# Kernel optimization log

Hardware: AMD Instinct MI355X
Metric: run time of the kernel (lower is better)

Reference implementation:

```python
import jax, jax.numpy as jnp
import numpy as np

B, T, N, E, H, MAXD = 32, 128, 42, 256, 8, 7
DH = E // H


def _hand_edges():
    left = [(0, 1), (1, 2), (2, 3), (3, 4), (0, 5), (5, 6), (6, 7), (7, 8), (0, 9), (9, 10), (10, 11), (11, 12), (0, 13), (13, 14), (14, 15), (15, 16), (0, 17), (17, 18), (18, 19), (19, 20)]
    right = [(21, 22), (22, 23), (23, 24), (24, 25), (21, 26), (26, 27), (27, 28), (28, 29), (21, 30), (30, 31), (31, 32), (32, 33), (21, 34), (34, 35), (35, 36), (36, 37), (21, 38), (38, 39), (39, 40), (40, 41)]
    tips = [(4, 8), (8, 12), (12, 16), (16, 20), (25, 29), (29, 33), (33, 37), (37, 41)]
    cross = [(0, 21)]
    return left + right + cross + tips


def _graph_constants():
    adj = np.zeros((N, N), dtype=np.float32)
    dist = np.zeros((N, N), dtype=np.float64)
    for a, b in _hand_edges():
        adj[a, b] = 1.0
        adj[b, a] = 1.0
        dist[a, b] = 1.0
        dist[b, a] = 1.0
    # exact replica of the module's single-pass Floyd-Warshall-style loop
    for k in range(N):
        for i in range(N):
            for j in range(N):
                if i != j and dist[i, k] > 0 and dist[k, j] > 0:
                    nd = dist[i, k] + dist[k, j]
                    if dist[i, j] == 0 or nd < dist[i, j]:
                        dist[i, j] = nd
    dist = np.clip(dist, 0, MAXD).astype(np.int32)
    return adj, dist


def setup_inputs() -> dict:
    key = jax.random.key(0)
    ks = jax.random.split(key, 12)
    adj_np, dist_np = _graph_constants()
    s_in = 1.0 / np.sqrt(E)
    return {
        'node_features': jax.random.normal(ks[0], (B, T, N, E), dtype=jnp.float32),
        'adjacency_matrix': jnp.asarray(adj_np),
        'distances': jnp.asarray(dist_np),
        'Wq': jax.random.normal(ks[1], (E, E), dtype=jnp.float32) * s_in,
        'bq': jnp.zeros((E,), dtype=jnp.float32),
        'Wk': jax.random.normal(ks[2], (E, E), dtype=jnp.float32) * s_in,
        'bk': jnp.zeros((E,), dtype=jnp.float32),
        'Wv': jax.random.normal(ks[3], (E, E), dtype=jnp.float32) * s_in,
        'bv': jnp.zeros((E,), dtype=jnp.float32),
        'Wo': jax.random.normal(ks[4], (E, E), dtype=jnp.float32) * s_in,
        'bo': jnp.zeros((E,), dtype=jnp.float32),
        'rel_emb': jax.random.normal(ks[5], (2 * MAXD + 1, H), dtype=jnp.float32) * 0.05,
    }


def reference(node_features, adjacency_matrix, distances, Wq, bq, Wk, bk, Wv, bv, Wo, bo, rel_emb):
    b, t, n, e = node_features.shape
    q = (node_features @ Wq + bq).reshape(b, t, n, H, DH)
    k = (node_features @ Wk + bk).reshape(b, t, n, H, DH)
    v = (node_features @ Wv + bv).reshape(b, t, n, H, DH)
    # scores: [b, t, h, i, j]
    scores = jnp.einsum('btihd,btjhd->bthij', q, k) / jnp.sqrt(jnp.float32(DH))
    # relative position bias: [n, n, h] -> [h, n, n]
    bias = rel_emb[distances]  # (N, N, H)
    scores = scores + jnp.transpose(bias, (2, 0, 1))[None, None]
    mask = (adjacency_matrix > 0).astype(jnp.float32)[None, None, None]
    scores = scores * mask + (1.0 - mask) * (-1e9)
    attn = jax.nn.softmax(scores, axis=-1)
    out = jnp.einsum('bthij,btjhd->btihd', attn, v).reshape(b, t, n, e)
    out = out @ Wo + bo
    return out, attn
```

## Files before the change

### kernel.cpp

```cpp
#include <hip/hip_runtime.h>
#include <stdint.h>


#define TPB 512
constexpr int BT = 4096;
constexpr int N = 42, NP = 48, E = 256, H = 8, DH = 32;
constexpr int NE = N * E;
constexpr int NN = N * N;
constexpr float SCALE = 0.17677669529663687f;

typedef short sh8 __attribute__((ext_vector_type(8)));
typedef float f4 __attribute__((ext_vector_type(4)));

__device__ __forceinline__ float b2f(uint16_t u) {
  union { uint32_t i; float f; } v; v.i = ((uint32_t)u) << 16; return v.f;
}
__device__ __forceinline__ uint16_t f2b(float f) {
  union { float f; uint32_t i; } v; v.f = f;
  const uint32_t x = v.i;
  return (uint16_t)((x + 0x7fffu + ((x >> 16) & 1u)) >> 16);
}

#define SWZ(base, row, cb) \
  ((char*)(base) + ((((row) << 9) + (cb)) ^ (((row) & 7) << 4)))

__global__ __launch_bounds__(256) void wt_kernel(
    const float* __restrict__ Wq, const float* __restrict__ Wk,
    const float* __restrict__ Wv, const float* __restrict__ Wo,
    uint16_t* __restrict__ WT) {
  __shared__ float tl[32][33];
  const int z = blockIdx.z;
  const float* W = (z == 0) ? Wq : (z == 1) ? Wk : (z == 2) ? Wv : Wo;
  uint16_t* dst = WT + z * 65536;
  const int k0 = blockIdx.y * 32, n0 = blockIdx.x * 32;
  const int r = threadIdx.x >> 5, cc = threadIdx.x & 31;
#pragma unroll
  for (int p = 0; p < 4; ++p)
    tl[r + 8 * p][cc] = W[(k0 + r + 8 * p) * E + n0 + cc];
  __syncthreads();
#pragma unroll
  for (int p = 0; p < 4; ++p)
    dst[(n0 + r + 8 * p) * E + k0 + cc] = f2b(tl[cc][r + 8 * p]);
}

__global__ __launch_bounds__(TPB, 2) void gt_kernel(
    const float* __restrict__ X, const float* __restrict__ adj,
    const int* __restrict__ dist,
    const float* __restrict__ bq, const float* __restrict__ bk,
    const float* __restrict__ bv, const float* __restrict__ bo,
    const float* __restrict__ rel, const uint16_t* __restrict__ WT,
    float* __restrict__ out, float* __restrict__ attn) {
  alignas(16) __shared__ uint16_t Xb[NP * E];
  alignas(16) __shared__ uint16_t Qb[NP * E];
  alignas(16) __shared__ uint16_t Kb[NP * E];
  alignas(16) __shared__ uint16_t VT[E * 56];
  alignas(16) __shared__ uint16_t Ps[8 * NP * 56];
  __shared__ uint8_t dm8[NP * NP];
  __shared__ float relL[120];

  const int gid = blockIdx.x;
  const int tid = threadIdx.x;
  const int w = tid >> 6, lane = tid & 63, c = lane & 15, lg = lane >> 4;

  const uint16_t* WTq = WT;
  const uint16_t* WTk = WT + 65536;
  const uint16_t* WTv = WT + 131072;
  const uint16_t* WTo = WT + 196608;

  {
    const float2* Xs = (const float2*)(X + (size_t)gid * NE);
    for (int i = tid; i < NE / 2; i += TPB) {
      const float2 v = Xs[i];
      const int row = i >> 7, cb = (i & 127) << 2;
      const uint32_t pk = (uint32_t)f2b(v.x) | ((uint32_t)f2b(v.y) << 16);
      *(uint32_t*)SWZ(Xb, row, cb) = pk;
    }
    for (int i = tid; i < (NP - N) * 128; i += TPB) {
      const int row = N + (i >> 7), cb = (i & 127) << 2;
      *(uint32_t*)SWZ(Xb, row, cb) = 0u;
    }
    for (int t = tid; t < NP * NP; t += TPB) {
      const int i = t / NP, j = t - i * NP;
      uint8_t v = 0;
      if (i < N && j < N) {
        const float a = adj[i * N + j];
        const int d = dist[i * N + j];
        v = (uint8_t)d | (a > 0.f ? 0x80 : 0);
      }
      dm8[t] = v;
    }
    for (int t = tid; t < 120; t += TPB) relL[t] = rel[t];
  }
  __syncthreads();

  const int nt0 = 2 * w;
  f4 aQ[3][2], aK[3][2], aV[3][2];
#pragma unroll
  for (int mt = 0; mt < 3; ++mt)
#pragma unroll
    for (int nt = 0; nt < 2; ++nt) {
      aQ[mt][nt] = (f4){0.f, 0.f, 0.f, 0.f};
      aK[mt][nt] = (f4){0.f, 0.f, 0.f, 0.f};
      aV[mt][nt] = (f4){0.f, 0.f, 0.f, 0.f};
    }
  for (int kc = 0; kc < E; kc += 32) {
    sh8 xa[3];
#pragma unroll
    for (int mt = 0; mt < 3; ++mt)
      xa[mt] = *(const sh8*)SWZ(Xb, 16 * mt + c, (kc + 8 * lg) * 2);
#pragma unroll
    for (int nt = 0; nt < 2; ++nt) {
      const int n = (nt0 + nt) * 16 + c;
      const int ko = n * E + kc + 8 * lg;
      const sh8 bq8 = *(const sh8*)(WTq + ko);
      const sh8 bk8 = *(const sh8*)(WTk + ko);
      const sh8 bv8 = *(const sh8*)(WTv + ko);
#pragma unroll
      for (int mt = 0; mt < 3; ++mt) {
        aQ[mt][nt] = __builtin_amdgcn_mfma_f32_16x16x32_bf16(xa[mt], bq8, aQ[mt][nt], 0, 0, 0);
        aK[mt][nt] = __builtin_amdgcn_mfma_f32_16x16x32_bf16(xa[mt], bk8, aK[mt][nt], 0, 0, 0);
        aV[mt][nt] = __builtin_amdgcn_mfma_f32_16x16x32_bf16(xa[mt], bv8, aV[mt][nt], 0, 0, 0);
      }
    }
  }
#pragma unroll
  for (int nt = 0; nt < 2; ++nt) {
    const int n = (nt0 + nt) * 16 + c;
    const float bqv = bq[n], bkv = bk[n], bvv = bv[n];
#pragma unroll
    for (int mt = 0; mt < 3; ++mt) {
      uint16_t vr[4];
#pragma unroll
      for (int r = 0; r < 4; ++r) {
        const int i = 16 * mt + 4 * lg + r;
        *(uint16_t*)SWZ(Qb, i, n * 2) = f2b(aQ[mt][nt][r] + bqv);
        *(uint16_t*)SWZ(Kb, i, n * 2) = f2b(aK[mt][nt][r] + bkv);
        vr[r] = f2b(aV[mt][nt][r] + bvv);
      }
      ushort4 vv; vv.x = vr[0]; vv.y = vr[1]; vv.z = vr[2]; vv.w = vr[3];
      *(ushort4*)(VT + n * 56 + 16 * mt + 4 * lg) = vv;
    }
  }
  __syncthreads();

  {
    const int h = w;
    sh8 qa[3], kb8[3];
#pragma unroll
    for (int t = 0; t < 3; ++t) {
      qa[t] = *(const sh8*)SWZ(Qb, 16 * t + c, (h * 32 + 8 * lg) * 2);
      kb8[t] = *(const sh8*)SWZ(Kb, 16 * t + c, (h * 32 + 8 * lg) * 2);
    }
    f4 st[3][3];
#pragma unroll
    for (int mt = 0; mt < 3; ++mt)
#pragma unroll
      for (int nt = 0; nt < 3; ++nt) {
        st[mt][nt] = (f4){0.f, 0.f, 0.f, 0.f};
        st[mt][nt] = __builtin_amdgcn_mfma_f32_16x16x32_bf16(qa[mt], kb8[nt], st[mt][nt], 0, 0, 0);
      }

    const size_t abase = ((size_t)gid * H + h) * (size_t)NN;
    uint16_t* Psw = Ps + w * NP * 56;
#pragma unroll
    for (int mt = 0; mt < 3; ++mt)
#pragma unroll
      for (int r = 0; r < 4; ++r) {
        const int i = 16 * mt + 4 * lg + r;
        float sv[3];
#pragma unroll
        for (int nt = 0; nt < 3; ++nt) {
          const int j = 16 * nt + c;
          const uint8_t dm = dm8[i * NP + j];
          sv[nt] = (dm & 0x80) ? st[mt][nt][r] * SCALE + relL[(dm & 0x7f) * 8 + h]
                               : -1e9f;
        }
        float m = fmaxf(fmaxf(sv[0], sv[1]), sv[2]);
        m = fmaxf(m, __shfl_xor(m, 1));
        m = fmaxf(m, __shfl_xor(m, 2));
        m = fmaxf(m, __shfl_xor(m, 4));
        m = fmaxf(m, __shfl_xor(m, 8));
        float p0 = __expf(sv[0] - m), p1 = __expf(sv[1] - m), p2 = __expf(sv[2] - m);
        float sum = p0 + p1 + p2;
        sum += __shfl_xor(sum, 1);
        sum += __shfl_xor(sum, 2);
        sum += __shfl_xor(sum, 4);
        sum += __shfl_xor(sum, 8);
        const float inv = __builtin_amdgcn_rcpf(sum);
        p0 *= inv; p1 *= inv; p2 *= inv;
        const float pv[3] = {p0, p1, p2};
#pragma unroll
        for (int nt = 0; nt < 3; ++nt) {
          const int j = 16 * nt + c;
          if (i < N && j < N) attn[abase + i * N + j] = pv[nt];
          Psw[i * 56 + j] = f2b(pv[nt]);
        }
      }

    const sh8 z8 = {0, 0, 0, 0, 0, 0, 0, 0};
    sh8 pa0[3], pa1[3], vb0[2], vb1[2];
#pragma unroll
    for (int mt = 0; mt < 3; ++mt) {
      pa0[mt] = *(const sh8*)(Psw + (16 * mt + c) * 56 + 8 * lg);
      pa1[mt] = (lg < 2) ? *(const sh8*)(Psw + (16 * mt + c) * 56 + 32 + 8 * lg) : z8;
    }
#pragma unroll
    for (int nt = 0; nt < 2; ++nt) {
      const int d = h * 32 + 16 * nt + c;
      vb0[nt] = *(const sh8*)(VT + d * 56 + 8 * lg);
      vb1[nt] = (lg < 2) ? *(const sh8*)(VT + d * 56 + 32 + 8 * lg) : z8;
    }
    f4 ov[3][2];
#pragma unroll
    for (int mt = 0; mt < 3; ++mt)
#pragma unroll
      for (int nt = 0; nt < 2; ++nt) {
        ov[mt][nt] = (f4){0.f, 0.f, 0.f, 0.f};
        ov[mt][nt] = __builtin_amdgcn_mfma_f32_16x16x32_bf16(pa0[mt], vb0[nt], ov[mt][nt], 0, 0, 0);
        ov[mt][nt] = __builtin_amdgcn_mfma_f32_16x16x32_bf16(pa1[mt], vb1[nt], ov[mt][nt], 0, 0, 0);
      }
#pragma unroll
    for (int mt = 0; mt < 3; ++mt)
#pragma unroll
      for (int nt = 0; nt < 2; ++nt)
#pragma unroll
        for (int r = 0; r < 4; ++r) {
          const int i = 16 * mt + 4 * lg + r;
          const int dn = h * 32 + 16 * nt + c;
          *(uint16_t*)SWZ(Xb, i, dn * 2) = f2b(ov[mt][nt][r]);
        }
  }
  __syncthreads();

  {
    f4 ao[3][2];
#pragma unroll
    for (int mt = 0; mt < 3; ++mt)
#pragma unroll
      for (int nt = 0; nt < 2; ++nt) ao[mt][nt] = (f4){0.f, 0.f, 0.f, 0.f};
    for (int kc = 0; kc < E; kc += 32) {
      sh8 xa[3];
#pragma unroll
      for (int mt = 0; mt < 3; ++mt)
        xa[mt] = *(const sh8*)SWZ(Xb, 16 * mt + c, (kc + 8 * lg) * 2);
#pragma unroll
      for (int nt = 0; nt < 2; ++nt) {
        const int n = (nt0 + nt) * 16 + c;
        const sh8 b8 = *(const sh8*)(WTo + n * E + kc + 8 * lg);
#pragma unroll
        for (int mt = 0; mt < 3; ++mt)
          ao[mt][nt] = __builtin_amdgcn_mfma_f32_16x16x32_bf16(xa[mt], b8, ao[mt][nt], 0, 0, 0);
      }
    }
#pragma unroll
    for (int nt = 0; nt < 2; ++nt) {
      const int n = (nt0 + nt) * 16 + c;
      const float bov = bo[n];
#pragma unroll
      for (int mt = 0; mt < 3; ++mt)
#pragma unroll
        for (int r = 0; r < 4; ++r) {
          const int i = 16 * mt + 4 * lg + r;
          if (i < N) out[(size_t)gid * NE + i * E + n] = ao[mt][nt][r] + bov;
        }
    }
  }
}

extern "C" void kernel_launch(void* const* d_in, const int* in_sizes, int n_in,
                              void* d_out, int out_size, void* d_ws, size_t ws_size,
                              hipStream_t stream) {
  const float* X    = (const float*)d_in[0];
  const float* adj  = (const float*)d_in[1];
  const int*   dist = (const int*)d_in[2];
  const float* Wq   = (const float*)d_in[3];
  const float* bq   = (const float*)d_in[4];
  const float* Wk   = (const float*)d_in[5];
  const float* bk   = (const float*)d_in[6];
  const float* Wv   = (const float*)d_in[7];
  const float* bv   = (const float*)d_in[8];
  const float* Wo   = (const float*)d_in[9];
  const float* bo   = (const float*)d_in[10];
  const float* rel  = (const float*)d_in[11];
  float* out  = (float*)d_out;
  float* attn = out + (size_t)BT * NE;
  uint16_t* WT = (uint16_t*)d_ws;

  wt_kernel<<<dim3(8, 8, 4), dim3(256), 0, stream>>>(Wq, Wk, Wv, Wo, WT);
  gt_kernel<<<dim3(BT), dim3(TPB), 0, stream>>>(
      X, adj, dist, bq, bk, bv, bo, rel, WT, out, attn);
}
```

Measured before the change: 543.3 us.

## Alias shared memory buffers to fit more blocks per CU and coalesce attn writes

Replaces the separate shared arrays with one aliased buffer. Xb overlaps VT, and Qb overlaps Ps, so LDS use drops to about 76 KB, and launch bounds are raised to 4 blocks per CU. Extra barriers are added where aliased regions are reused. The attention-probability store now writes contiguous rows per wave from the bf16 LDS copy instead of scattered per-fragment fp32 stores. That makes the attn output bf16-rounded, and the higher occupancy target may cap registers and cause spills.

```diff
diff --git a/kernel.cpp b/kernel.cpp
--- a/kernel.cpp
+++ b/kernel.cpp
@@ -43,20 +43,21 @@
     dst[(n0 + r + 8 * p) * E + k0 + cc] = f2b(tl[cc][r + 8 * p]);
 }
 
-__global__ __launch_bounds__(TPB, 2) void gt_kernel(
+__global__ __launch_bounds__(TPB, 4) void gt_kernel(
     const float* __restrict__ X, const float* __restrict__ adj,
     const int* __restrict__ dist,
     const float* __restrict__ bq, const float* __restrict__ bk,
     const float* __restrict__ bv, const float* __restrict__ bo,
     const float* __restrict__ rel, const uint16_t* __restrict__ WT,
     float* __restrict__ out, float* __restrict__ attn) {
-  alignas(16) __shared__ uint16_t Xb[NP * E];
-  alignas(16) __shared__ uint16_t Qb[NP * E];
-  alignas(16) __shared__ uint16_t Kb[NP * E];
-  alignas(16) __shared__ uint16_t VT[E * 56];
-  alignas(16) __shared__ uint16_t Ps[8 * NP * 56];
-  __shared__ uint8_t dm8[NP * NP];
-  __shared__ float relL[120];
+  alignas(16) __shared__ char smem[76512];
+  uint16_t* const Xb = (uint16_t*)smem;
+  uint16_t* const VT = (uint16_t*)smem;
+  uint16_t* const Qb = (uint16_t*)(smem + 24576);
+  uint16_t* const Kb = (uint16_t*)(smem + 49152);
+  uint16_t* const Ps = (uint16_t*)(smem + 24576);
+  uint8_t*  const dm8 = (uint8_t*)(smem + 73728);
+  float*    const relL = (float*)(smem + 76032);
 
   const int gid = blockIdx.x;
   const int tid = threadIdx.x;
@@ -123,6 +124,8 @@
       }
     }
   }
+  __syncthreads();
+
 #pragma unroll
   for (int nt = 0; nt < 2; ++nt) {
     const int n = (nt0 + nt) * 16 + c;
@@ -138,7 +141,7 @@
         vr[r] = f2b(aV[mt][nt][r] + bvv);
       }
       ushort4 vv; vv.x = vr[0]; vv.y = vr[1]; vv.z = vr[2]; vv.w = vr[3];
-      *(ushort4*)(VT + n * 56 + 16 * mt + 4 * lg) = vv;
+      *(ushort4*)(VT + n * 48 + 16 * mt + 4 * lg) = vv;
     }
   }
   __syncthreads();
@@ -151,6 +154,8 @@
       qa[t] = *(const sh8*)SWZ(Qb, 16 * t + c, (h * 32 + 8 * lg) * 2);
       kb8[t] = *(const sh8*)SWZ(Kb, 16 * t + c, (h * 32 + 8 * lg) * 2);
     }
+    __syncthreads();
+
     f4 st[3][3];
 #pragma unroll
     for (int mt = 0; mt < 3; ++mt)
@@ -160,8 +165,7 @@
         st[mt][nt] = __builtin_amdgcn_mfma_f32_16x16x32_bf16(qa[mt], kb8[nt], st[mt][nt], 0, 0, 0);
       }
 
-    const size_t abase = ((size_t)gid * H + h) * (size_t)NN;
-    uint16_t* Psw = Ps + w * NP * 56;
+    uint16_t* Psw = Ps + w * 2688;
 #pragma unroll
     for (int mt = 0; mt < 3; ++mt)
 #pragma unroll
@@ -187,15 +191,18 @@
         sum += __shfl_xor(sum, 4);
         sum += __shfl_xor(sum, 8);
         const float inv = __builtin_amdgcn_rcpf(sum);
-        p0 *= inv; p1 *= inv; p2 *= inv;
-        const float pv[3] = {p0, p1, p2};
-#pragma unroll
-        for (int nt = 0; nt < 3; ++nt) {
-          const int j = 16 * nt + c;
-          if (i < N && j < N) attn[abase + i * N + j] = pv[nt];
-          Psw[i * 56 + j] = f2b(pv[nt]);
-        }
-      }
+        Psw[i * 56 + 16 * 0 + c] = f2b(p0 * inv);
+        Psw[i * 56 + 16 * 1 + c] = f2b(p1 * inv);
+        Psw[i * 56 + 16 * 2 + c] = f2b(p2 * inv);
+      }
+
+    {
+      const size_t abase = ((size_t)gid * H + h) * (size_t)NN;
+      for (int p = lane; p < NN; p += 64) {
+        const int i = p / N, j = p - i * N;
+        attn[abase + p] = b2f(Psw[i * 56 + j]);
+      }
+    }
 
     const sh8 z8 = {0, 0, 0, 0, 0, 0, 0, 0};
     sh8 pa0[3], pa1[3], vb0[2], vb1[2];
@@ -207,8 +214,8 @@
 #pragma unroll
     for (int nt = 0; nt < 2; ++nt) {
       const int d = h * 32 + 16 * nt + c;
-      vb0[nt] = *(const sh8*)(VT + d * 56 + 8 * lg);
-      vb1[nt] = (lg < 2) ? *(const sh8*)(VT + d * 56 + 32 + 8 * lg) : z8;
+      vb0[nt] = *(const sh8*)(VT + d * 48 + 8 * lg);
+      vb1[nt] = (lg < 2) ? *(const sh8*)(VT + d * 48 + 32 + 8 * lg) : z8;
     }
     f4 ov[3][2];
 #pragma unroll
@@ -219,6 +226,7 @@
         ov[mt][nt] = __builtin_amdgcn_mfma_f32_16x16x32_bf16(pa0[mt], vb0[nt], ov[mt][nt], 0, 0, 0);
         ov[mt][nt] = __builtin_amdgcn_mfma_f32_16x16x32_bf16(pa1[mt], vb1[nt], ov[mt][nt], 0, 0, 0);
       }
+    __syncthreads();
 #pragma unroll
     for (int mt = 0; mt < 3; ++mt)
 #pragma unroll
```

Result: faster. 439.6 us (-19.1%).
